# Optimization experiments

Measured on AMD Instinct MI355X. Metric: run time of the kernel, lower is better.

## Reference

```python
import jax, jax.numpy as jnp
import numpy as np

KERNEL_MUL = 2.0
KERNEL_NUM = 5


def _mmd_rbf(x_src, x_tar):
    b = x_src.shape[0]
    total = jnp.concatenate([x_src, x_tar], axis=0)          # [2N, D]
    n = total.shape[0]
    # pairwise squared L2 distances via ||a||^2 + ||b||^2 - 2 a.b (same math,
    # avoids the O(n^2 * D) broadcasted intermediate of the torch code)
    sq = jnp.sum(total * total, axis=-1)                      # [2N]
    L2 = sq[:, None] + sq[None, :] - 2.0 * (total @ total.T)  # [2N, 2N]
    L2 = jnp.maximum(L2, 0.0)
    # bandwidth from .data -> no gradient flows through it
    bandwidth = jax.lax.stop_gradient(jnp.sum(L2)) / (n * n - n)
    bandwidth = bandwidth / (KERNEL_MUL ** (KERNEL_NUM // 2))
    kernels = jnp.zeros_like(L2)
    for i in range(KERNEL_NUM):
        kernels = kernels + jnp.exp(-L2 / (bandwidth * (KERNEL_MUL ** i)))
    XX = kernels[:b, :b]
    YY = kernels[b:, b:]
    XY = kernels[:b, b:]
    YX = kernels[b:, :b]
    return jnp.mean(XX + YY - XY - YX)


def setup_inputs() -> dict:
    key = jax.random.key(0)
    k1, k2 = jax.random.split(key)
    x_src = jax.random.normal(k1, (4096, 256), dtype=jnp.float32)
    x_tar = jax.random.normal(k2, (4096, 256), dtype=jnp.float32)
    return {"x_src": x_src, "x_tar": x_tar}


def reference(x_src, x_tar):
    return _mmd_rbf(x_src, x_tar)
```

## Files before the change

### kernel.cpp

```cpp
#include <hip/hip_runtime.h>

#define D      256
#define NROWS  8192
#define BHALF  4096
#define TILE   128
#define NT2    (NROWS / TILE)
#define NBLK   (NT2 * (NT2 + 1) / 2)
#define NGRID  512
#define NBINS  64
#define QS     25.0f

typedef __attribute__((ext_vector_type(4))) int i32x4;

#if __has_builtin(__builtin_amdgcn_exp2f)
#define EXP2F(x) __builtin_amdgcn_exp2f(x)
#else
#define EXP2F(x) exp2f(x)
#endif


__device__ __forceinline__ int q8(float x) {
    return (int)__builtin_rintf(fminf(fmaxf(x * QS, -127.f), 127.f));
}

__device__ __forceinline__ void gload_lds16(const signed char* g, signed char* l) {
    __builtin_amdgcn_global_load_lds(
        (const __attribute__((address_space(1))) unsigned int*)g,
        (__attribute__((address_space(3))) unsigned int*)l,
        16, 0, 0);
}

__global__ __launch_bounds__(256)
void pre_kernel(const float* __restrict__ src, const float* __restrict__ tar,
                float* __restrict__ sq, float* __restrict__ colsum,
                double* __restrict__ sumsq, signed char* __restrict__ Ti) {
    __shared__ float cs[D];
    int t = threadIdx.x;
    cs[t] = 0.f;
    __syncthreads();

    int lane = t & 63, w = t >> 6;
    int rowBase = blockIdx.x * 32 + w * 8;

    float4 v[8];
    #pragma unroll
    for (int it = 0; it < 8; ++it) {
        int r = rowBase + it;
        const float* rowp = (r < BHALF) ? (src + (size_t)r * D)
                                        : (tar + (size_t)(r - BHALF) * D);
        v[it] = *(const float4*)(rowp + lane * 4);
    }

    float4 csum = make_float4(0.f, 0.f, 0.f, 0.f);
    float sqacc = 0.f;
    #pragma unroll
    for (int it = 0; it < 8; ++it) {
        int r = rowBase + it;
        int q0 = q8(v[it].x), q1 = q8(v[it].y), q2 = q8(v[it].z), q3 = q8(v[it].w);
        unsigned pk = (unsigned)(q0 & 255) | ((unsigned)(q1 & 255) << 8) |
                      ((unsigned)(q2 & 255) << 16) | ((unsigned)(q3 & 255) << 24);
        *(unsigned*)(Ti + (size_t)r * D + lane * 4) = pk;
        csum.x += v[it].x; csum.y += v[it].y; csum.z += v[it].z; csum.w += v[it].w;
        float s = v[it].x * v[it].x + v[it].y * v[it].y +
                  v[it].z * v[it].z + v[it].w * v[it].w;
        #pragma unroll
        for (int off = 32; off; off >>= 1) s += __shfl_xor(s, off, 64);
        if (lane == 0) { sq[r] = s; sqacc += s; }
    }
    atomicAdd(&cs[lane * 4 + 0], csum.x);
    atomicAdd(&cs[lane * 4 + 1], csum.y);
    atomicAdd(&cs[lane * 4 + 2], csum.z);
    atomicAdd(&cs[lane * 4 + 3], csum.w);
    if (lane == 0) atomicAdd(sumsq, (double)sqacc);
    __syncthreads();
    atomicAdd(&colsum[t], cs[t]);
}

__global__ __launch_bounds__(256, 2)
void mmd_main(const signed char* __restrict__ Ti,
              const float* __restrict__ sq, const float* __restrict__ colsum,
              const double* __restrict__ sumsq,
              double* __restrict__ bins, unsigned* __restrict__ counter,
              float* __restrict__ out)
{
    __shared__ signed char As[TILE * D];
    __shared__ signed char Bs[TILE * D];

    int t = threadIdx.x, lane = t & 63, wid = t >> 6;
    int wi = wid >> 1, wj = wid & 1;
    int lr = lane & 15, lk = lane >> 4;

    int bid = blockIdx.x;
    int sw = (bid & 7) * (NGRID / 8) + (bid >> 3);
    int pstart = (int)(((long)sw * NBLK) / NGRID);
    int pend   = (int)(((long)(sw + 1) * NBLK) / NGRID);

    int ti, tj;
    {
        int rem = pstart, a = 0;
        while (rem >= NT2 - a) { rem -= NT2 - a; ++a; }
        ti = a; tj = a + rem;
    }

    auto stage = [&](signed char* dst, int tt) {
        const signed char* g = Ti + (size_t)tt * TILE * D;
        #pragma unroll
        for (int p = 0; p < 8; ++p) {
            int q = p * 256 + t;
            int row = q >> 4, c = q & 15;
            gload_lds16(g + row * D + ((c ^ (row & 7)) << 4), dst + (q << 4));
        }
    };

    stage(As, ti);
    stage(Bs, tj);

    float4 c4 = *(const float4*)(colsum + lane * 4);
    float s = c4.x * c4.x + c4.y * c4.y + c4.z * c4.z + c4.w * c4.w;
    #pragma unroll
    for (int off = 32; off; off >>= 1) s += __shfl_xor(s, off, 64);
    double sumL2 = 2.0 * (double)NROWS * (*sumsq) - 2.0 * (double)s;
    double bwd = sumL2 / ((double)NROWS * (double)NROWS - (double)NROWS) / 4.0;
    float g2 = (float)(1.4426950408889634 / (16.0 * bwd));
    float c2 = 2.f * g2 / (QS * QS);

    float running = 0.f;

    for (int p = pstart; p < pend; ++p) {
        int rowA = ti * TILE + wi * 64, rowB = tj * TILE + wj * 64;
        float gsj[4], gsi[4][4];
        #pragma unroll
        for (int n = 0; n < 4; ++n) gsj[n] = g2 * sq[rowB + n * 16 + lr];
        #pragma unroll
        for (int m = 0; m < 4; ++m)
            #pragma unroll
            for (int r = 0; r < 4; ++r)
                gsi[m][r] = g2 * sq[rowA + m * 16 + lk * 4 + r];

        asm volatile("s_waitcnt vmcnt(0)" ::: "memory");
        __syncthreads();

        i32x4 acc[4][4];
        #pragma unroll
        for (int m = 0; m < 4; ++m)
            #pragma unroll
            for (int n = 0; n < 4; ++n)
                acc[m][n] = (i32x4){0, 0, 0, 0};

        #pragma unroll
        for (int ks = 0; ks < 4; ++ks) {
            i32x4 av[4], bv[4];
            int ca = ks * 4 + lk;
            #pragma unroll
            for (int m = 0; m < 4; ++m) {
                int rA = wi * 64 + m * 16 + lr;
                av[m] = *(const i32x4*)&As[rA * D + ((ca ^ (rA & 7)) << 4)];
            }
            #pragma unroll
            for (int n = 0; n < 4; ++n) {
                int rB = wj * 64 + n * 16 + lr;
                bv[n] = *(const i32x4*)&Bs[rB * D + ((ca ^ (rB & 7)) << 4)];
            }
            #pragma unroll
            for (int m = 0; m < 4; ++m)
                #pragma unroll
                for (int n = 0; n < 4; ++n)
                    acc[m][n] = __builtin_amdgcn_mfma_i32_16x16x64_i8(
                                    av[m], bv[n], acc[m][n], 0, 0, 0);
        }
        __syncthreads();

        int nti = ti, ntj = tj + 1;
        if (ntj >= NT2) { nti = ti + 1; ntj = nti; }
        if (p + 1 < pend) {
            stage(Bs, ntj);
            if (nti != ti) stage(As, nti);
        }

        bool strad = (ti == tj);
        float lanesum = 0.f;
        #pragma unroll
        for (int m = 0; m < 4; ++m) {
            #pragma unroll
            for (int r = 0; r < 4; ++r) {
                float gi_s = gsi[m][r];
                #pragma unroll
                for (int n = 0; n < 4; ++n) {
                    float fd = (float)acc[m][n][r];
                    float e  = fminf(fmaf(c2, fd, -(gi_s + gsj[n])), 0.f);
                    float uu = EXP2F(e);
                    float u2 = uu * uu, u4 = u2 * u2, u8 = u4 * u4, u16 = u8 * u8;
                    float s5 = uu + u2 + u4 + u8 + u16;
                    if (strad) {
                        int gi = rowA + m * 16 + lk * 4 + r;
                        int gj = rowB + n * 16 + lr;
                        float w = (gj > gi) ? 2.f : ((gj == gi) ? 1.f : 0.f);
                        lanesum = fmaf(w, s5, lanesum);
                    } else {
                        lanesum += s5;
                    }
                }
            }
        }
        float sgn = ((ti < NT2 / 2) == (tj < NT2 / 2)) ? 1.f : -1.f;
        running = fmaf(strad ? sgn : 2.f * sgn, lanesum, running);

        ti = nti; tj = ntj;
    }

    #pragma unroll
    for (int off = 32; off; off >>= 1) running += __shfl_xor(running, off, 64);
    if (lane == 0)
        atomicAdd(&bins[((sw << 2) + wid) & (NBINS - 1)], (double)running);

    __syncthreads();
    if (t == 0) {
        __threadfence();
        unsigned old = atomicAdd(counter, 1u);
        if (old == NGRID - 1) {
            __threadfence();
            double tot = 0.0;
            for (int i = 0; i < NBINS; ++i)
                tot += ((volatile double*)bins)[i];
            out[0] = (float)(tot / ((double)BHALF * (double)BHALF));
        }
    }
}

extern "C" void kernel_launch(void* const* d_in, const int* in_sizes, int n_in,
                              void* d_out, int out_size, void* d_ws, size_t ws_size,
                              hipStream_t stream) {
    const float* src = (const float*)d_in[0];
    const float* tar = (const float*)d_in[1];
    float* out = (float*)d_out;

    char* ws = (char*)d_ws;
    double*   sumsq   = (double*)(ws + 0);
    unsigned* counter = (unsigned*)(ws + 8);
    double*   bins    = (double*)(ws + 16);
    float*    colsum  = (float*)(ws + 1024);
    float*    sq      = (float*)(ws + 4096);
    signed char* Ti   = (signed char*)(ws + 36864);

    hipMemsetAsync(ws, 0, 2048, stream);
    pre_kernel<<<256, 256, 0, stream>>>(src, tar, sq, colsum, sumsq, Ti);
    mmd_main<<<NGRID, 256, 0, stream>>>(Ti, sq, colsum, sumsq, bins, counter, out);
}
```

Measured before the change: 115.2 us.

## Fuse preprocessing into main kernel with a software grid barrier

Merges the quantize/norm pre-pass into the main MFMA kernel. Each of the 512 blocks now handles 16 rows of the pre-pass, then all blocks spin on a global ready counter before the tiled int8 pairwise pass begins. This removes one kernel launch and the gap between the two kernels. It also defers the per-row squared-norm loads until after the MMA loop and reloads the A-side norms only when the row tile changes. The grid barrier relies on all 512 blocks being co-resident (2 per CU by launch bounds), and it adds spin-wait overhead.

```diff
diff --git a/kernel.cpp b/kernel.cpp
--- a/kernel.cpp
+++ b/kernel.cpp
@@ -30,58 +30,12 @@
         16, 0, 0);
 }
 
-__global__ __launch_bounds__(256)
-void pre_kernel(const float* __restrict__ src, const float* __restrict__ tar,
-                float* __restrict__ sq, float* __restrict__ colsum,
-                double* __restrict__ sumsq, signed char* __restrict__ Ti) {
-    __shared__ float cs[D];
-    int t = threadIdx.x;
-    cs[t] = 0.f;
-    __syncthreads();
-
-    int lane = t & 63, w = t >> 6;
-    int rowBase = blockIdx.x * 32 + w * 8;
-
-    float4 v[8];
-    #pragma unroll
-    for (int it = 0; it < 8; ++it) {
-        int r = rowBase + it;
-        const float* rowp = (r < BHALF) ? (src + (size_t)r * D)
-                                        : (tar + (size_t)(r - BHALF) * D);
-        v[it] = *(const float4*)(rowp + lane * 4);
-    }
-
-    float4 csum = make_float4(0.f, 0.f, 0.f, 0.f);
-    float sqacc = 0.f;
-    #pragma unroll
-    for (int it = 0; it < 8; ++it) {
-        int r = rowBase + it;
-        int q0 = q8(v[it].x), q1 = q8(v[it].y), q2 = q8(v[it].z), q3 = q8(v[it].w);
-        unsigned pk = (unsigned)(q0 & 255) | ((unsigned)(q1 & 255) << 8) |
-                      ((unsigned)(q2 & 255) << 16) | ((unsigned)(q3 & 255) << 24);
-        *(unsigned*)(Ti + (size_t)r * D + lane * 4) = pk;
-        csum.x += v[it].x; csum.y += v[it].y; csum.z += v[it].z; csum.w += v[it].w;
-        float s = v[it].x * v[it].x + v[it].y * v[it].y +
-                  v[it].z * v[it].z + v[it].w * v[it].w;
-        #pragma unroll
-        for (int off = 32; off; off >>= 1) s += __shfl_xor(s, off, 64);
-        if (lane == 0) { sq[r] = s; sqacc += s; }
-    }
-    atomicAdd(&cs[lane * 4 + 0], csum.x);
-    atomicAdd(&cs[lane * 4 + 1], csum.y);
-    atomicAdd(&cs[lane * 4 + 2], csum.z);
-    atomicAdd(&cs[lane * 4 + 3], csum.w);
-    if (lane == 0) atomicAdd(sumsq, (double)sqacc);
-    __syncthreads();
-    atomicAdd(&colsum[t], cs[t]);
-}
-
 __global__ __launch_bounds__(256, 2)
-void mmd_main(const signed char* __restrict__ Ti,
-              const float* __restrict__ sq, const float* __restrict__ colsum,
-              const double* __restrict__ sumsq,
-              double* __restrict__ bins, unsigned* __restrict__ counter,
-              float* __restrict__ out)
+void mmd_fused(const float* __restrict__ src, const float* __restrict__ tar,
+               signed char* __restrict__ Ti, float* __restrict__ sq,
+               float* __restrict__ colsum, double* __restrict__ sumsq,
+               double* __restrict__ bins, unsigned* __restrict__ counter,
+               unsigned* __restrict__ ready, float* __restrict__ out)
 {
     __shared__ signed char As[TILE * D];
     __shared__ signed char Bs[TILE * D];
@@ -89,31 +43,57 @@
     int t = threadIdx.x, lane = t & 63, wid = t >> 6;
     int wi = wid >> 1, wj = wid & 1;
     int lr = lane & 15, lk = lane >> 4;
-
     int bid = blockIdx.x;
-    int sw = (bid & 7) * (NGRID / 8) + (bid >> 3);
-    int pstart = (int)(((long)sw * NBLK) / NGRID);
-    int pend   = (int)(((long)(sw + 1) * NBLK) / NGRID);
-
-    int ti, tj;
+
     {
-        int rem = pstart, a = 0;
-        while (rem >= NT2 - a) { rem -= NT2 - a; ++a; }
-        ti = a; tj = a + rem;
-    }
-
-    auto stage = [&](signed char* dst, int tt) {
-        const signed char* g = Ti + (size_t)tt * TILE * D;
-        #pragma unroll
-        for (int p = 0; p < 8; ++p) {
-            int q = p * 256 + t;
-            int row = q >> 4, c = q & 15;
-            gload_lds16(g + row * D + ((c ^ (row & 7)) << 4), dst + (q << 4));
-        }
-    };
-
-    stage(As, ti);
-    stage(Bs, tj);
+        float* cs = (float*)As;
+        cs[t] = 0.f;
+        __syncthreads();
+
+        int rowBase = bid * 16 + wid * 4;
+        float4 v[4];
+        #pragma unroll
+        for (int it = 0; it < 4; ++it) {
+            int r = rowBase + it;
+            const float* rowp = (r < BHALF) ? (src + (size_t)r * D)
+                                            : (tar + (size_t)(r - BHALF) * D);
+            v[it] = *(const float4*)(rowp + lane * 4);
+        }
+        float4 csum = make_float4(0.f, 0.f, 0.f, 0.f);
+        float sqacc = 0.f;
+        #pragma unroll
+        for (int it = 0; it < 4; ++it) {
+            int r = rowBase + it;
+            int q0 = q8(v[it].x), q1 = q8(v[it].y), q2 = q8(v[it].z), q3 = q8(v[it].w);
+            unsigned pk = (unsigned)(q0 & 255) | ((unsigned)(q1 & 255) << 8) |
+                          ((unsigned)(q2 & 255) << 16) | ((unsigned)(q3 & 255) << 24);
+            *(unsigned*)(Ti + (size_t)r * D + lane * 4) = pk;
+            csum.x += v[it].x; csum.y += v[it].y; csum.z += v[it].z; csum.w += v[it].w;
+            float s = v[it].x * v[it].x + v[it].y * v[it].y +
+                      v[it].z * v[it].z + v[it].w * v[it].w;
+            #pragma unroll
+            for (int off = 32; off; off >>= 1) s += __shfl_xor(s, off, 64);
+            if (lane == 0) { sq[r] = s; sqacc += s; }
+        }
+        atomicAdd(&cs[lane * 4 + 0], csum.x);
+        atomicAdd(&cs[lane * 4 + 1], csum.y);
+        atomicAdd(&cs[lane * 4 + 2], csum.z);
+        atomicAdd(&cs[lane * 4 + 3], csum.w);
+        if (lane == 0) atomicAdd(sumsq, (double)sqacc);
+        __syncthreads();
+        atomicAdd(&colsum[t], cs[t]);
+        __syncthreads();
+
+        if (t == 0) {
+            __threadfence();
+            atomicAdd(ready, 1u);
+            while (__hip_atomic_load(ready, __ATOMIC_ACQUIRE,
+                                     __HIP_MEMORY_SCOPE_AGENT) < NGRID)
+                __builtin_amdgcn_s_sleep(2);
+            __threadfence();
+        }
+        __syncthreads();
+    }
 
     float4 c4 = *(const float4*)(colsum + lane * 4);
     float s = c4.x * c4.x + c4.y * c4.y + c4.z * c4.z + c4.w * c4.w;
@@ -124,19 +104,35 @@
     float g2 = (float)(1.4426950408889634 / (16.0 * bwd));
     float c2 = 2.f * g2 / (QS * QS);
 
+    int sw = (bid & 7) * (NGRID / 8) + (bid >> 3);
+    int pstart = (int)(((long)sw * NBLK) / NGRID);
+    int pend   = (int)(((long)(sw + 1) * NBLK) / NGRID);
+
+    int ti, tj;
+    {
+        int rem = pstart, a = 0;
+        while (rem >= NT2 - a) { rem -= NT2 - a; ++a; }
+        ti = a; tj = a + rem;
+    }
+
+    auto stage = [&](signed char* dst, int tt) {
+        const signed char* g = Ti + (size_t)tt * TILE * D;
+        #pragma unroll
+        for (int p = 0; p < 8; ++p) {
+            int q = p * 256 + t;
+            int row = q >> 4, c = q & 15;
+            gload_lds16(g + row * D + ((c ^ (row & 7)) << 4), dst + (q << 4));
+        }
+    };
+
+    stage(As, ti);
+    stage(Bs, tj);
+
+    float gsi[4][4], gsj[4];
+    int gsiA = -1;
     float running = 0.f;
 
     for (int p = pstart; p < pend; ++p) {
-        int rowA = ti * TILE + wi * 64, rowB = tj * TILE + wj * 64;
-        float gsj[4], gsi[4][4];
-        #pragma unroll
-        for (int n = 0; n < 4; ++n) gsj[n] = g2 * sq[rowB + n * 16 + lr];
-        #pragma unroll
-        for (int m = 0; m < 4; ++m)
-            #pragma unroll
-            for (int r = 0; r < 4; ++r)
-                gsi[m][r] = g2 * sq[rowA + m * 16 + lk * 4 + r];
-
         asm volatile("s_waitcnt vmcnt(0)" ::: "memory");
         __syncthreads();
 
@@ -176,6 +172,18 @@
             stage(Bs, ntj);
             if (nti != ti) stage(As, nti);
         }
+
+        int rowA = ti * TILE + wi * 64, rowB = tj * TILE + wj * 64;
+        if (ti != gsiA) {
+            #pragma unroll
+            for (int m = 0; m < 4; ++m)
+                #pragma unroll
+                for (int r = 0; r < 4; ++r)
+                    gsi[m][r] = g2 * sq[rowA + m * 16 + lk * 4 + r];
+            gsiA = ti;
+        }
+        #pragma unroll
+        for (int n = 0; n < 4; ++n) gsj[n] = g2 * sq[rowB + n * 16 + lr];
 
         bool strad = (ti == tj);
         float lanesum = 0.f;
@@ -237,12 +245,13 @@
     char* ws = (char*)d_ws;
     double*   sumsq   = (double*)(ws + 0);
     unsigned* counter = (unsigned*)(ws + 8);
+    unsigned* ready   = (unsigned*)(ws + 12);
     double*   bins    = (double*)(ws + 16);
     float*    colsum  = (float*)(ws + 1024);
     float*    sq      = (float*)(ws + 4096);
     signed char* Ti   = (signed char*)(ws + 36864);
 
     hipMemsetAsync(ws, 0, 2048, stream);
-    pre_kernel<<<256, 256, 0, stream>>>(src, tar, sq, colsum, sumsq, Ti);
-    mmd_main<<<NGRID, 256, 0, stream>>>(Ti, sq, colsum, sumsq, bins, counter, out);
-}
+    mmd_fused<<<NGRID, 256, 0, stream>>>(src, tar, Ti, sq, colsum, sumsq,
+                                         bins, counter, ready, out);
+}
```

New measurement: 150.3 us. +30.5%, slower.

## Split B tiles to 64 rows with double-buffered LDS and prefetched row norms

Applied to the files above, without the earlier changes.

The 128x128 output tile becomes 128x64. Each of the four waves now owns 32 rows and all 64 columns, and the triangular pair enumeration is rewritten for the rectangular tile grid. B tiles are double-buffered in LDS so the next B tile can load while the current one is consumed. The next tile's squared-norm values are fetched before the exp epilogue rather than at the top of the loop. The intent is finer load balance across blocks, less wasted work on the diagonal, and a shorter serial path per step. The cost is fewer MFMAs per LDS fragment load and more loop iterations, each with its own sync.

```diff
diff --git a/kernel.cpp b/kernel.cpp
--- a/kernel.cpp
+++ b/kernel.cpp
@@ -3,9 +3,11 @@
 #define D      256
 #define NROWS  8192
 #define BHALF  4096
-#define TILE   128
-#define NT2    (NROWS / TILE)
-#define NBLK   (NT2 * (NT2 + 1) / 2)
+#define TA     128
+#define TB     64
+#define NTA    (NROWS / TA)
+#define NTB    (NROWS / TB)
+#define NPAIR  4160
 #define NGRID  512
 #define NBINS  64
 #define QS     25.0f
@@ -83,37 +85,45 @@
               double* __restrict__ bins, unsigned* __restrict__ counter,
               float* __restrict__ out)
 {
-    __shared__ signed char As[TILE * D];
-    __shared__ signed char Bs[TILE * D];
+    __shared__ signed char As[TA * D];
+    __shared__ signed char Bs[2][TB * D];
 
     int t = threadIdx.x, lane = t & 63, wid = t >> 6;
-    int wi = wid >> 1, wj = wid & 1;
     int lr = lane & 15, lk = lane >> 4;
 
     int bid = blockIdx.x;
     int sw = (bid & 7) * (NGRID / 8) + (bid >> 3);
-    int pstart = (int)(((long)sw * NBLK) / NGRID);
-    int pend   = (int)(((long)(sw + 1) * NBLK) / NGRID);
+    int pstart = (int)(((long)sw * NPAIR) / NGRID);
+    int pend   = (int)(((long)(sw + 1) * NPAIR) / NGRID);
 
     int ti, tj;
     {
         int rem = pstart, a = 0;
-        while (rem >= NT2 - a) { rem -= NT2 - a; ++a; }
-        ti = a; tj = a + rem;
-    }
-
-    auto stage = [&](signed char* dst, int tt) {
-        const signed char* g = Ti + (size_t)tt * TILE * D;
+        while (rem >= NTB - 2 * a) { rem -= NTB - 2 * a; ++a; }
+        ti = a; tj = 2 * a + rem;
+    }
+
+    auto stageA = [&](int tt) {
+        const signed char* g = Ti + (size_t)tt * TA * D;
         #pragma unroll
         for (int p = 0; p < 8; ++p) {
             int q = p * 256 + t;
             int row = q >> 4, c = q & 15;
-            gload_lds16(g + row * D + ((c ^ (row & 7)) << 4), dst + (q << 4));
+            gload_lds16(g + row * D + ((c ^ (row & 7)) << 4), As + (q << 4));
         }
     };
-
-    stage(As, ti);
-    stage(Bs, tj);
+    auto stageB = [&](int buf, int tt) {
+        const signed char* g = Ti + (size_t)tt * TB * D;
+        #pragma unroll
+        for (int p = 0; p < 4; ++p) {
+            int q = p * 256 + t;
+            int row = q >> 4, c = q & 15;
+            gload_lds16(g + row * D + ((c ^ (row & 7)) << 4), Bs[buf] + (q << 4));
+        }
+    };
+
+    stageA(ti);
+    stageB(0, tj);
 
     float4 c4 = *(const float4*)(colsum + lane * 4);
     float s = c4.x * c4.x + c4.y * c4.y + c4.z * c4.z + c4.w * c4.w;
@@ -124,45 +134,45 @@
     float g2 = (float)(1.4426950408889634 / (16.0 * bwd));
     float c2 = 2.f * g2 / (QS * QS);
 
+    float gsi[2][4], gsj[4];
+    #pragma unroll
+    for (int m = 0; m < 2; ++m)
+        #pragma unroll
+        for (int r = 0; r < 4; ++r)
+            gsi[m][r] = g2 * sq[ti * TA + wid * 32 + m * 16 + lk * 4 + r];
+    #pragma unroll
+    for (int n = 0; n < 4; ++n) gsj[n] = g2 * sq[tj * TB + n * 16 + lr];
+
     float running = 0.f;
+    int cur = 0;
 
     for (int p = pstart; p < pend; ++p) {
-        int rowA = ti * TILE + wi * 64, rowB = tj * TILE + wj * 64;
-        float gsj[4], gsi[4][4];
-        #pragma unroll
-        for (int n = 0; n < 4; ++n) gsj[n] = g2 * sq[rowB + n * 16 + lr];
-        #pragma unroll
-        for (int m = 0; m < 4; ++m)
-            #pragma unroll
-            for (int r = 0; r < 4; ++r)
-                gsi[m][r] = g2 * sq[rowA + m * 16 + lk * 4 + r];
-
         asm volatile("s_waitcnt vmcnt(0)" ::: "memory");
         __syncthreads();
 
-        i32x4 acc[4][4];
-        #pragma unroll
-        for (int m = 0; m < 4; ++m)
+        i32x4 acc[2][4];
+        #pragma unroll
+        for (int m = 0; m < 2; ++m)
             #pragma unroll
             for (int n = 0; n < 4; ++n)
                 acc[m][n] = (i32x4){0, 0, 0, 0};
 
         #pragma unroll
         for (int ks = 0; ks < 4; ++ks) {
-            i32x4 av[4], bv[4];
+            i32x4 av[2], bv[4];
             int ca = ks * 4 + lk;
             #pragma unroll
-            for (int m = 0; m < 4; ++m) {
-                int rA = wi * 64 + m * 16 + lr;
+            for (int m = 0; m < 2; ++m) {
+                int rA = wid * 32 + m * 16 + lr;
                 av[m] = *(const i32x4*)&As[rA * D + ((ca ^ (rA & 7)) << 4)];
             }
             #pragma unroll
             for (int n = 0; n < 4; ++n) {
-                int rB = wj * 64 + n * 16 + lr;
-                bv[n] = *(const i32x4*)&Bs[rB * D + ((ca ^ (rB & 7)) << 4)];
-            }
-            #pragma unroll
-            for (int m = 0; m < 4; ++m)
+                int rB = n * 16 + lr;
+                bv[n] = *(const i32x4*)&Bs[cur][rB * D + ((ca ^ (rB & 7)) << 4)];
+            }
+            #pragma unroll
+            for (int m = 0; m < 2; ++m)
                 #pragma unroll
                 for (int n = 0; n < 4; ++n)
                     acc[m][n] = __builtin_amdgcn_mfma_i32_16x16x64_i8(
@@ -171,16 +181,32 @@
         __syncthreads();
 
         int nti = ti, ntj = tj + 1;
-        if (ntj >= NT2) { nti = ti + 1; ntj = nti; }
+        if (ntj >= NTB) { ++nti; ntj = 2 * nti; }
+        float ngsi[2][4], ngsj[4];
         if (p + 1 < pend) {
-            stage(Bs, ntj);
-            if (nti != ti) stage(As, nti);
-        }
-
-        bool strad = (ti == tj);
+            stageB(cur ^ 1, ntj);
+            if (nti != ti) stageA(nti);
+            if (nti != ti) {
+                #pragma unroll
+                for (int m = 0; m < 2; ++m)
+                    #pragma unroll
+                    for (int r = 0; r < 4; ++r)
+                        ngsi[m][r] = g2 * sq[nti * TA + wid * 32 + m * 16 + lk * 4 + r];
+            } else {
+                #pragma unroll
+                for (int m = 0; m < 2; ++m)
+                    #pragma unroll
+                    for (int r = 0; r < 4; ++r)
+                        ngsi[m][r] = gsi[m][r];
+            }
+            #pragma unroll
+            for (int n = 0; n < 4; ++n) ngsj[n] = g2 * sq[ntj * TB + n * 16 + lr];
+        }
+
+        bool strad = ((tj >> 1) == ti);
         float lanesum = 0.f;
         #pragma unroll
-        for (int m = 0; m < 4; ++m) {
+        for (int m = 0; m < 2; ++m) {
             #pragma unroll
             for (int r = 0; r < 4; ++r) {
                 float gi_s = gsi[m][r];
@@ -192,8 +218,8 @@
                     float u2 = uu * uu, u4 = u2 * u2, u8 = u4 * u4, u16 = u8 * u8;
                     float s5 = uu + u2 + u4 + u8 + u16;
                     if (strad) {
-                        int gi = rowA + m * 16 + lk * 4 + r;
-                        int gj = rowB + n * 16 + lr;
+                        int gi = ti * TA + wid * 32 + m * 16 + lk * 4 + r;
+                        int gj = tj * TB + n * 16 + lr;
                         float w = (gj > gi) ? 2.f : ((gj == gi) ? 1.f : 0.f);
                         lanesum = fmaf(w, s5, lanesum);
                     } else {
@@ -202,10 +228,18 @@
                 }
             }
         }
-        float sgn = ((ti < NT2 / 2) == (tj < NT2 / 2)) ? 1.f : -1.f;
+        float sgn = ((ti < NTA / 2) == (tj < NTB / 2)) ? 1.f : -1.f;
         running = fmaf(strad ? sgn : 2.f * sgn, lanesum, running);
 
-        ti = nti; tj = ntj;
+        if (p + 1 < pend) {
+            #pragma unroll
+            for (int m = 0; m < 2; ++m)
+                #pragma unroll
+                for (int r = 0; r < 4; ++r) gsi[m][r] = ngsi[m][r];
+            #pragma unroll
+            for (int n = 0; n < 4; ++n) gsj[n] = ngsj[n];
+        }
+        ti = nti; tj = ntj; cur ^= 1;
     }
 
     #pragma unroll
```

Measured after the change: 114.9 us. Within noise of the previous version (-0.3%).
